# Optimization experiments

Hardware: AMD Instinct MI355X
Metric: run time of the kernel (lower is better)

Reference implementation:

```python
import jax, jax.numpy as jnp
import numpy as np

D_MODEL = 1024
NUM_HEADS = 16
D_K = D_MODEL // NUM_HEADS

def setup_inputs() -> dict:
    key = jax.random.key(0)
    ks = jax.random.split(key, 8)
    B, S, D = 2, 2048, D_MODEL
    scale = 1.0 / np.sqrt(D)
    return {
        "X_q": jax.random.normal(ks[0], (B, S, D), dtype=jnp.float32),
        "X_k": jax.random.normal(ks[1], (B, S, D), dtype=jnp.float32),
        "X_v": jax.random.normal(ks[2], (B, S, D), dtype=jnp.float32),
        "W_q": jax.random.normal(ks[3], (D, D), dtype=jnp.float32) * scale,
        "W_k": jax.random.normal(ks[4], (D, D), dtype=jnp.float32) * scale,
        "W_v": jax.random.normal(ks[5], (D, D), dtype=jnp.float32) * scale,
        "W_o": jax.random.normal(ks[6], (D, D), dtype=jnp.float32) * scale,
        "b_o": jnp.zeros((D,), dtype=jnp.float32),
    }

def reference(X_q, X_k, X_v, W_q, W_k, W_v, W_o, b_o):
    B, S, D = X_q.shape
    H, dk = NUM_HEADS, D_K
    # nn.Linear: x @ W.T
    Q = (X_q @ W_q.T).reshape(B, H, S, dk)  # faithful raw view, no transpose
    K = (X_k @ W_k.T).reshape(B, H, S, dk)
    V = (X_v @ W_v.T).reshape(B, H, S, dk)
    A = jnp.einsum("bhqd,bhkd->bhqk", Q, K) / np.sqrt(dk)  # [B,H,S,S]
    A = jax.nn.softmax(A, axis=-1)
    H_cat = jnp.einsum("bhqk,bhkd->bhqd", A, V).reshape(B, S, D)
    return H_cat @ W_o.T + b_o
```

## Files before the change

### kernel.cpp

```cpp
#include <hip/hip_runtime.h>

typedef __bf16 bf16;
typedef bf16 bf16x8 __attribute__((ext_vector_type(8)));
typedef bf16 bf16x4 __attribute__((ext_vector_type(4)));
typedef bf16 bf16x2 __attribute__((ext_vector_type(2)));
typedef float f32x4 __attribute__((ext_vector_type(4)));
typedef float f32x16 __attribute__((ext_vector_type(16)));
typedef int i32x4 __attribute__((ext_vector_type(4)));

#define XSZ 4194304
#define WSZ 1048576
#define KDIM 1024
#define QSCALE 0.1803368801111137f

__device__ __forceinline__ void async16(const bf16* g, bf16* l) {
  __builtin_amdgcn_global_load_lds(
      (const __attribute__((address_space(1))) unsigned int*)g,
      (__attribute__((address_space(3))) unsigned int*)l, 16, 0, 0);
}

__device__ __forceinline__ bf16x8 ld8(const bf16* p) {
  bf16x4 lo = *(const bf16x4*)p;
  bf16x4 hi = *(const bf16x4*)(p + 4);
  return __builtin_shufflevector(lo, hi, 0, 1, 2, 3, 4, 5, 6, 7);
}

__device__ __forceinline__ void st8s(bf16* p, bf16x8 v) {
  *(bf16x4*)p       = __builtin_shufflevector(v, v, 0, 1, 2, 3);
  *(bf16x4*)(p + 4) = __builtin_shufflevector(v, v, 4, 5, 6, 7);
}

__device__ __forceinline__ f32x4 mfma16(bf16x8 a, bf16x8 b, f32x4 c) {
  return __builtin_amdgcn_mfma_f32_16x16x32_bf16(a, b, c, 0, 0, 0);
}
__device__ __forceinline__ f32x16 mfma32(bf16x8 a, bf16x8 b, f32x16 c) {
  return __builtin_amdgcn_mfma_f32_32x32x16_bf16(a, b, c, 0, 0, 0);
}

__device__ __forceinline__ int packbf2(float lo, float hi) {
  bf16x2 t; t[0] = (bf16)lo; t[1] = (bf16)hi;
  return __builtin_bit_cast(int, t);
}

__device__ __forceinline__ float fast_exp2(float x) {
#if __has_builtin(__builtin_amdgcn_exp2f)
  return __builtin_amdgcn_exp2f(x);
#else
  return exp2f(x);
#endif
}

__global__ __launch_bounds__(256) void cast_all(const float* __restrict__ Xq, const float* __restrict__ Xk,
                                                const float* __restrict__ Xv, const float* __restrict__ Wq,
                                                const float* __restrict__ Wk, const float* __restrict__ Wv,
                                                const float* __restrict__ Wo, bf16* __restrict__ dst) {
  size_t i = ((size_t)blockIdx.x * 256 + threadIdx.x) * 8;
  const float* src; size_t off; float scale = 1.0f;
  if (i < XSZ)                { src = Xq; off = i; }
  else if (i < 2 * (size_t)XSZ) { src = Xk; off = i - XSZ; }
  else if (i < 3 * (size_t)XSZ) { src = Xv; off = i - 2 * (size_t)XSZ; }
  else if (i < 3 * (size_t)XSZ + WSZ) { src = Wq; off = i - 3 * (size_t)XSZ; scale = QSCALE; }
  else if (i < 3 * (size_t)XSZ + 2 * (size_t)WSZ) { src = Wk; off = i - 3 * (size_t)XSZ - WSZ; }
  else if (i < 3 * (size_t)XSZ + 3 * (size_t)WSZ) { src = Wv; off = i - 3 * (size_t)XSZ - 2 * (size_t)WSZ; }
  else                        { src = Wo; off = i - 3 * (size_t)XSZ - 3 * (size_t)WSZ; }
  float4 a = *(const float4*)(src + off);
  float4 b = *(const float4*)(src + off + 4);
  bf16x8 o;
  o[0] = (bf16)(a.x * scale); o[1] = (bf16)(a.y * scale);
  o[2] = (bf16)(a.z * scale); o[3] = (bf16)(a.w * scale);
  o[4] = (bf16)(b.x * scale); o[5] = (bf16)(b.y * scale);
  o[6] = (bf16)(b.z * scale); o[7] = (bf16)(b.w * scale);
  *(bf16x8*)(dst + i) = o;
}

__device__ __forceinline__ void gemm_nt_core(const bf16* __restrict__ A, const bf16* __restrict__ Bm,
                                             int m0, int n0, bf16* lds, f32x4 acc[4][4]) {
  const int t = threadIdx.x;
  const int lane = t & 63, wave = t >> 6;
  const int wm = wave & 1, wn = wave >> 1;
  const int quad = lane >> 4, m16 = lane & 15;
  bf16* As = lds;
  bf16* Bs = lds + 128 * 32;
  const int c0 = t, c1 = t + 256;
  const bf16* ga0 = A + (size_t)(m0 + (c0 >> 2)) * KDIM + (c0 & 3) * 8;
  const bf16* ga1 = A + (size_t)(m0 + (c1 >> 2)) * KDIM + (c1 & 3) * 8;
  const bf16* gb0 = Bm + (size_t)(n0 + (c0 >> 2)) * KDIM + (c0 & 3) * 8;
  const bf16* gb1 = Bm + (size_t)(n0 + (c1 >> 2)) * KDIM + (c1 & 3) * 8;
  for (int kt = 0; kt < KDIM; kt += 32) {
    async16(ga0 + kt, As + c0 * 8);
    async16(ga1 + kt, As + c1 * 8);
    async16(gb0 + kt, Bs + c0 * 8);
    async16(gb1 + kt, Bs + c1 * 8);
    __syncthreads();
    bf16x8 af[4], bfv[4];
    #pragma unroll
    for (int i = 0; i < 4; i++)
      af[i] = *(const bf16x8*)(As + (wm * 64 + i * 16 + m16) * 32 + quad * 8);
    #pragma unroll
    for (int i = 0; i < 4; i++)
      bfv[i] = *(const bf16x8*)(Bs + (wn * 64 + i * 16 + m16) * 32 + quad * 8);
    #pragma unroll
    for (int mi = 0; mi < 4; mi++)
      #pragma unroll
      for (int ni = 0; ni < 4; ni++)
        acc[mi][ni] = mfma16(af[mi], bfv[ni], acc[mi][ni]);
    __syncthreads();
  }
}

__global__ __launch_bounds__(256) void proj_gemm(const bf16* __restrict__ xq, const bf16* __restrict__ xk,
                                                 const bf16* __restrict__ xv, const bf16* __restrict__ wq,
                                                 const bf16* __restrict__ wk, const bf16* __restrict__ wv,
                                                 bf16* __restrict__ Qo, bf16* __restrict__ Ko,
                                                 bf16* __restrict__ Vo) {
  __shared__ bf16 lds[2 * 128 * 32];
  const int z = blockIdx.z;
  const bf16* A = (z == 0) ? xq : (z == 1) ? xk : xv;
  const bf16* W = (z == 0) ? wq : (z == 1) ? wk : wv;
  bf16* C = (z == 0) ? Qo : (z == 1) ? Ko : Vo;
  f32x4 acc[4][4];
  #pragma unroll
  for (int i = 0; i < 4; i++)
    #pragma unroll
    for (int j = 0; j < 4; j++) acc[i][j] = (f32x4){0.f, 0.f, 0.f, 0.f};
  gemm_nt_core(A, W, blockIdx.y * 128, blockIdx.x * 128, lds, acc);
  const int lane = threadIdx.x & 63, wave = threadIdx.x >> 6;
  const int wm = wave & 1, wn = wave >> 1, quad = lane >> 4, m16 = lane & 15;
  const int row0 = blockIdx.y * 128 + wm * 64;
  const int col0 = blockIdx.x * 128 + wn * 64;
  #pragma unroll
  for (int mi = 0; mi < 4; mi++)
    #pragma unroll
    for (int ni = 0; ni < 4; ni++)
      #pragma unroll
      for (int r = 0; r < 4; r++) {
        int row = row0 + mi * 16 + quad * 4 + r;
        int col = col0 + ni * 16 + m16;
        C[(size_t)row * 1024 + col] = (bf16)acc[mi][ni][r];
      }
}

__global__ __launch_bounds__(256) void out_gemm(const bf16* __restrict__ Hm, const bf16* __restrict__ wo,
                                                const float* __restrict__ bias, float* __restrict__ out) {
  __shared__ bf16 lds[128 * 32 + 64 * 32];
  bf16* As = lds;
  bf16* Bs = lds + 128 * 32;
  const int t = threadIdx.x;
  const int lane = t & 63, wave = t >> 6;
  const int wm = wave & 1, wn = wave >> 1;
  const int quad = lane >> 4, m16 = lane & 15;
  const int m0 = blockIdx.y * 128, n0 = blockIdx.x * 64;
  const int c0 = t, c1 = t + 256;
  const bf16* ga0 = Hm + (size_t)(m0 + (c0 >> 2)) * KDIM + (c0 & 3) * 8;
  const bf16* ga1 = Hm + (size_t)(m0 + (c1 >> 2)) * KDIM + (c1 & 3) * 8;
  const bf16* gb0 = wo + (size_t)(n0 + (c0 >> 2)) * KDIM + (c0 & 3) * 8;
  f32x4 acc[4][2];
  #pragma unroll
  for (int i = 0; i < 4; i++)
    #pragma unroll
    for (int j = 0; j < 2; j++) acc[i][j] = (f32x4){0.f, 0.f, 0.f, 0.f};
  for (int kt = 0; kt < KDIM; kt += 32) {
    async16(ga0 + kt, As + c0 * 8);
    async16(ga1 + kt, As + c1 * 8);
    if (c0 < 256) async16(gb0 + kt, Bs + c0 * 8);
    __syncthreads();
    bf16x8 af[4], bfv[2];
    #pragma unroll
    for (int i = 0; i < 4; i++)
      af[i] = *(const bf16x8*)(As + (wm * 64 + i * 16 + m16) * 32 + quad * 8);
    #pragma unroll
    for (int i = 0; i < 2; i++)
      bfv[i] = *(const bf16x8*)(Bs + (wn * 32 + i * 16 + m16) * 32 + quad * 8);
    #pragma unroll
    for (int mi = 0; mi < 4; mi++)
      #pragma unroll
      for (int ni = 0; ni < 2; ni++)
        acc[mi][ni] = mfma16(af[mi], bfv[ni], acc[mi][ni]);
    __syncthreads();
  }
  const int row0 = m0 + wm * 64;
  const int col0 = n0 + wn * 32;
  float bv[2];
  #pragma unroll
  for (int ni = 0; ni < 2; ni++) bv[ni] = bias[col0 + ni * 16 + m16];
  #pragma unroll
  for (int mi = 0; mi < 4; mi++)
    #pragma unroll
    for (int ni = 0; ni < 2; ni++)
      #pragma unroll
      for (int r = 0; r < 4; r++) {
        int row = row0 + mi * 16 + quad * 4 + r;
        int col = col0 + ni * 16 + m16;
        out[(size_t)row * 1024 + col] = acc[mi][ni][r] + bv[ni];
      }
}

__global__ __launch_bounds__(256) void transpose_v(const bf16* __restrict__ V, bf16* __restrict__ Vt) {
  __shared__ bf16 T[64 * 65];
  const int t = threadIdx.x;
  const bf16* src = V + (size_t)blockIdx.y * (2048 * 64) + (size_t)blockIdx.x * 64 * 64;
  bf16* dst = Vt + (size_t)blockIdx.y * (2048 * 64) + (size_t)blockIdx.x * 64;
  #pragma unroll
  for (int j = 0; j < 2; j++) {
    int c = t + j * 256;
    int row = c >> 3, col8 = (c & 7) * 8;
    bf16x8 v = *(const bf16x8*)(src + row * 64 + col8);
    #pragma unroll
    for (int i = 0; i < 8; i++) T[row * 65 + col8 + i] = v[i];
  }
  __syncthreads();
  #pragma unroll
  for (int j = 0; j < 2; j++) {
    int c = t + j * 256;
    int d = c >> 3, k8 = (c & 7) * 8;
    bf16x8 o;
    #pragma unroll
    for (int i = 0; i < 8; i++) o[i] = T[(k8 + i) * 65 + d];
    *(bf16x8*)(dst + (size_t)d * 2048 + k8) = o;
  }
}

#define KS 68
#define VS 132
__global__ __launch_bounds__(256, 3) void attn_kernel(const bf16* __restrict__ Qg,
                                                      const bf16* __restrict__ Kg,
                                                      const bf16* __restrict__ Vtg,
                                                      float* __restrict__ U0,
                                                      float* __restrict__ l0) {
  __shared__ bf16 smem[128 * KS + 64 * VS];
  bf16* Ks = smem;
  bf16* Vs = smem + 128 * KS;
  const int t = threadIdx.x;
  const int lane = t & 63, w = t >> 6;
  const int l31 = lane & 31, h = lane >> 5;
  const int L = blockIdx.x + 16 * (blockIdx.y + 32 * blockIdx.z);
  const int xcd = L & 7, j5 = L >> 3;
  const int bh = xcd * 4 + (j5 & 3);
  const int slab = (j5 >> 2) & 1;
  const int qt = j5 >> 3;
  const size_t base = (size_t)bh * (2048 * 64);
  const bf16* Kp = Kg + base + (size_t)slab * (1024 * 64);
  const bf16* Vp = Vtg + base + slab * 1024;
  float* U = U0 + (size_t)slab * (32 * 131072) + (size_t)bh * 131072;
  float* lv = l0 + slab * (32 * 2048) + bh * 2048;
  const int q = qt * 128 + w * 32 + l31;

  bf16x8 qf[4];
  #pragma unroll
  for (int kc = 0; kc < 4; kc++)
    qf[kc] = *(const bf16x8*)(Qg + base + (size_t)q * 64 + 16 * kc + 8 * h);

  f32x16 oacc[2];
  #pragma unroll
  for (int mt = 0; mt < 2; mt++)
    #pragma unroll
    for (int i = 0; i < 16; i++) oacc[mt][i] = 0.f;
  float lrow = 0.f;

  int krow[4], kcol[4], vrow[4], vcol[4];
  #pragma unroll
  for (int j = 0; j < 4; j++) {
    int c = t + j * 256;
    krow[j] = c >> 3;  kcol[j] = (c & 7) * 8;
    vrow[j] = c >> 4;  vcol[j] = (c & 15) * 8;
  }

  bf16x8 kreg[4], vreg[4];
  #pragma unroll
  for (int j = 0; j < 4; j++) {
    kreg[j] = *(const bf16x8*)(Kp + (size_t)krow[j] * 64 + kcol[j]);
    vreg[j] = *(const bf16x8*)(Vp + (size_t)vrow[j] * 2048 + vcol[j]);
  }

  for (int kt = 0; kt < 8; kt++) {
    #pragma unroll
    for (int j = 0; j < 4; j++) st8s(Ks + krow[j] * KS + kcol[j], kreg[j]);
    #pragma unroll
    for (int j = 0; j < 4; j++) st8s(Vs + vrow[j] * VS + vcol[j], vreg[j]);
    __syncthreads();

    if (kt + 1 < 8) {
      #pragma unroll
      for (int j = 0; j < 4; j++) {
        kreg[j] = *(const bf16x8*)(Kp + (size_t)((kt + 1) * 128 + krow[j]) * 64 + kcol[j]);
        vreg[j] = *(const bf16x8*)(Vp + (size_t)vrow[j] * 2048 + (kt + 1) * 128 + vcol[j]);
      }
    }

    #pragma unroll
    for (int mt = 0; mt < 4; mt++) {
      f32x16 sacc;
      #pragma unroll
      for (int i = 0; i < 16; i++) sacc[i] = 0.f;
      #pragma unroll
      for (int kc = 0; kc < 4; kc++) {
        bf16x8 kf = ld8(Ks + (32 * mt + l31) * KS + 16 * kc + 8 * h);
        sacc = mfma32(kf, qf[kc], sacc);
      }
      int pd[8];
      float sum = 0.f;
      #pragma unroll
      for (int p = 0; p < 8; p++) {
        float p0 = fast_exp2(sacc[2 * p]);
        float p1 = fast_exp2(sacc[2 * p + 1]);
        sum += p0 + p1;
        pd[p] = packbf2(p0, p1);
      }
      lrow += sum;
      #pragma unroll
      for (int c1 = 0; c1 < 2; c1++) {
        const int kc = 2 * mt + c1;
        const int rro = 2 * c1 + h;
        const int rrp = 2 * c1 + 1 - h;
        int s0 = __shfl_xor(pd[2 * rrp], 32, 64);
        int s1 = __shfl_xor(pd[2 * rrp + 1], 32, 64);
        int o0 = pd[2 * rro], o1 = pd[2 * rro + 1];
        i32x4 w4;
        w4.x = h ? s0 : o0;
        w4.y = h ? s1 : o1;
        w4.z = h ? o0 : s0;
        w4.w = h ? o1 : s1;
        bf16x8 pfrag = __builtin_bit_cast(bf16x8, w4);
        #pragma unroll
        for (int mtd = 0; mtd < 2; mtd++) {
          bf16x8 vf = ld8(Vs + (32 * mtd + l31) * VS + 16 * kc + 8 * h);
          oacc[mtd] = mfma32(vf, pfrag, oacc[mtd]);
        }
      }
    }
    __syncthreads();
  }

  lrow += __shfl_xor(lrow, 32, 64);
  #pragma unroll
  for (int mt = 0; mt < 2; mt++)
    #pragma unroll
    for (int r = 0; r < 16; r++) {
      int d = 32 * mt + (r & 3) + 8 * (r >> 2) + 4 * h;
      U[(size_t)d * 2048 + q] = oacc[mt][r];
    }
  if (h == 0) lv[q] = lrow;
}

__global__ __launch_bounds__(256) void merge_kernel(const float* __restrict__ Ua,
                                                    const float* __restrict__ Ub,
                                                    const float* __restrict__ la,
                                                    const float* __restrict__ lb,
                                                    bf16* __restrict__ H) {
  __shared__ float T[64 * 65];
  const int t = threadIdx.x;
  const int q0 = blockIdx.x * 64;
  const int bh = blockIdx.y;
  const float* A = Ua + (size_t)bh * 131072;
  const float* Bp = Ub + (size_t)bh * 131072;
  #pragma unroll
  for (int p = 0; p < 4; p++) {
    int d = p * 16 + (t >> 4);
    int qq = (t & 15) * 4;
    f32x4 a = *(const f32x4*)(A + (size_t)d * 2048 + q0 + qq);
    f32x4 b = *(const f32x4*)(Bp + (size_t)d * 2048 + q0 + qq);
    #pragma unroll
    for (int i = 0; i < 4; i++) T[d * 65 + qq + i] = a[i] + b[i];
  }
  __syncthreads();
  const float* lap = la + bh * 2048 + q0;
  const float* lbp = lb + bh * 2048 + q0;
  #pragma unroll
  for (int p = 0; p < 2; p++) {
    int ql = p * 32 + (t >> 3);
    int d8 = (t & 7) * 8;
    float inv = 1.f / (lap[ql] + lbp[ql]);
    bf16x8 o;
    #pragma unroll
    for (int i = 0; i < 8; i++) o[i] = (bf16)(T[(d8 + i) * 65 + ql] * inv);
    *(bf16x8*)(H + (size_t)bh * 131072 + (size_t)(q0 + ql) * 64 + d8) = o;
  }
}

extern "C" void kernel_launch(void* const* d_in, const int* in_sizes, int n_in,
                              void* d_out, int out_size, void* d_ws, size_t ws_size,
                              hipStream_t stream) {
  const float* Xq = (const float*)d_in[0];
  const float* Xk = (const float*)d_in[1];
  const float* Xv = (const float*)d_in[2];
  const float* Wq = (const float*)d_in[3];
  const float* Wk = (const float*)d_in[4];
  const float* Wv = (const float*)d_in[5];
  const float* Wo = (const float*)d_in[6];
  const float* bo = (const float*)d_in[7];

  bf16* ws = (bf16*)d_ws;
  bf16* xq = ws;
  bf16* xk = ws + XSZ;
  bf16* xv = ws + 2 * (size_t)XSZ;
  bf16* wq = ws + 3 * (size_t)XSZ;
  bf16* wk = wq + WSZ;
  bf16* wv = wk + WSZ;
  bf16* wo = wv + WSZ;
  bf16* q  = wo + WSZ;
  bf16* k  = q + XSZ;
  bf16* v  = k + XSZ;
  bf16* vt = xv;
  bf16* h  = xq;
  float* U0  = (float*)v;
  float* l0f = (float*)xk;

  cast_all<<<8192, 256, 0, stream>>>(Xq, Xk, Xv, Wq, Wk, Wv, Wo, ws);
  proj_gemm<<<dim3(8, 32, 3), 256, 0, stream>>>(xq, xk, xv, wq, wk, wv, q, k, v);
  transpose_v<<<dim3(32, 32), 256, 0, stream>>>(v, vt);
  attn_kernel<<<dim3(16, 32, 2), 256, 0, stream>>>(q, k, vt, U0, l0f);
  merge_kernel<<<dim3(32, 32), 256, 0, stream>>>(U0, U0 + 32 * 131072, l0f, l0f + 65536, h);
  out_gemm<<<dim3(16, 32), 256, 0, stream>>>(h, wo, bo, (float*)d_out);
}
```

Baseline: 257.1 us.

## Process two query tiles per attention block to reuse K/V shared-memory tiles

Each attention block now handles 256 queries (two 128-query groups) instead of 128, so every K/V tile staged in LDS and every K/V fragment loaded into registers feeds twice as many MFMAs. The grid is halved and launch bounds drop from 3 to 2 blocks per CU to allow the larger register footprint. The intent is to cut global and LDS traffic per unit of compute, at the cost of fewer blocks (1024 vs 512 per slab set) and lower occupancy, which could hurt latency hiding.

```diff
diff --git a/kernel.cpp b/kernel.cpp
--- a/kernel.cpp
+++ b/kernel.cpp
@@ -222,7 +222,7 @@
 
 #define KS 68
 #define VS 132
-__global__ __launch_bounds__(256, 3) void attn_kernel(const bf16* __restrict__ Qg,
+__global__ __launch_bounds__(256, 2) void attn_kernel(const bf16* __restrict__ Qg,
                                                       const bf16* __restrict__ Kg,
                                                       const bf16* __restrict__ Vtg,
                                                       float* __restrict__ U0,
@@ -233,7 +233,7 @@
   const int t = threadIdx.x;
   const int lane = t & 63, w = t >> 6;
   const int l31 = lane & 31, h = lane >> 5;
-  const int L = blockIdx.x + 16 * (blockIdx.y + 32 * blockIdx.z);
+  const int L = blockIdx.x + 8 * (blockIdx.y + 32 * blockIdx.z);
   const int xcd = L & 7, j5 = L >> 3;
   const int bh = xcd * 4 + (j5 & 3);
   const int slab = (j5 >> 2) & 1;
@@ -243,19 +243,24 @@
   const bf16* Vp = Vtg + base + slab * 1024;
   float* U = U0 + (size_t)slab * (32 * 131072) + (size_t)bh * 131072;
   float* lv = l0 + slab * (32 * 2048) + bh * 2048;
-  const int q = qt * 128 + w * 32 + l31;
-
-  bf16x8 qf[4];
-  #pragma unroll
-  for (int kc = 0; kc < 4; kc++)
-    qf[kc] = *(const bf16x8*)(Qg + base + (size_t)q * 64 + 16 * kc + 8 * h);
-
-  f32x16 oacc[2];
-  #pragma unroll
-  for (int mt = 0; mt < 2; mt++)
-    #pragma unroll
-    for (int i = 0; i < 16; i++) oacc[mt][i] = 0.f;
-  float lrow = 0.f;
+  const int qc0 = qt * 256 + w * 32 + l31;
+  const int qc1 = qc0 + 128;
+
+  bf16x8 qf[2][4];
+  #pragma unroll
+  for (int kc = 0; kc < 4; kc++) {
+    qf[0][kc] = *(const bf16x8*)(Qg + base + (size_t)qc0 * 64 + 16 * kc + 8 * h);
+    qf[1][kc] = *(const bf16x8*)(Qg + base + (size_t)qc1 * 64 + 16 * kc + 8 * h);
+  }
+
+  f32x16 oacc[2][2];
+  #pragma unroll
+  for (int g = 0; g < 2; g++)
+    #pragma unroll
+    for (int mtd = 0; mtd < 2; mtd++)
+      #pragma unroll
+      for (int i = 0; i < 16; i++) oacc[g][mtd][i] = 0.f;
+  float lrow[2] = {0.f, 0.f};
 
   int krow[4], kcol[4], vrow[4], vcol[4];
   #pragma unroll
@@ -289,57 +294,69 @@
 
     #pragma unroll
     for (int mt = 0; mt < 4; mt++) {
-      f32x16 sacc;
-      #pragma unroll
-      for (int i = 0; i < 16; i++) sacc[i] = 0.f;
+      bf16x8 kf[4];
+      #pragma unroll
+      for (int kc = 0; kc < 4; kc++)
+        kf[kc] = ld8(Ks + (32 * mt + l31) * KS + 16 * kc + 8 * h);
+      f32x16 s0, s1;
+      #pragma unroll
+      for (int i = 0; i < 16; i++) { s0[i] = 0.f; s1[i] = 0.f; }
       #pragma unroll
       for (int kc = 0; kc < 4; kc++) {
-        bf16x8 kf = ld8(Ks + (32 * mt + l31) * KS + 16 * kc + 8 * h);
-        sacc = mfma32(kf, qf[kc], sacc);
-      }
-      int pd[8];
-      float sum = 0.f;
+        s0 = mfma32(kf[kc], qf[0][kc], s0);
+        s1 = mfma32(kf[kc], qf[1][kc], s1);
+      }
+      int pd[2][8];
+      float sum0 = 0.f, sum1 = 0.f;
       #pragma unroll
       for (int p = 0; p < 8; p++) {
-        float p0 = fast_exp2(sacc[2 * p]);
-        float p1 = fast_exp2(sacc[2 * p + 1]);
-        sum += p0 + p1;
-        pd[p] = packbf2(p0, p1);
-      }
-      lrow += sum;
+        float a0 = fast_exp2(s0[2 * p]), a1 = fast_exp2(s0[2 * p + 1]);
+        sum0 += a0 + a1;
+        pd[0][p] = packbf2(a0, a1);
+        float b0 = fast_exp2(s1[2 * p]), b1 = fast_exp2(s1[2 * p + 1]);
+        sum1 += b0 + b1;
+        pd[1][p] = packbf2(b0, b1);
+      }
+      lrow[0] += sum0; lrow[1] += sum1;
       #pragma unroll
       for (int c1 = 0; c1 < 2; c1++) {
         const int kc = 2 * mt + c1;
+        bf16x8 vf0 = ld8(Vs + (size_t)l31 * VS + 16 * kc + 8 * h);
+        bf16x8 vf1 = ld8(Vs + (size_t)(32 + l31) * VS + 16 * kc + 8 * h);
         const int rro = 2 * c1 + h;
         const int rrp = 2 * c1 + 1 - h;
-        int s0 = __shfl_xor(pd[2 * rrp], 32, 64);
-        int s1 = __shfl_xor(pd[2 * rrp + 1], 32, 64);
-        int o0 = pd[2 * rro], o1 = pd[2 * rro + 1];
-        i32x4 w4;
-        w4.x = h ? s0 : o0;
-        w4.y = h ? s1 : o1;
-        w4.z = h ? o0 : s0;
-        w4.w = h ? o1 : s1;
-        bf16x8 pfrag = __builtin_bit_cast(bf16x8, w4);
         #pragma unroll
-        for (int mtd = 0; mtd < 2; mtd++) {
-          bf16x8 vf = ld8(Vs + (32 * mtd + l31) * VS + 16 * kc + 8 * h);
-          oacc[mtd] = mfma32(vf, pfrag, oacc[mtd]);
+        for (int g = 0; g < 2; g++) {
+          int sw0 = __shfl_xor(pd[g][2 * rrp], 32, 64);
+          int sw1 = __shfl_xor(pd[g][2 * rrp + 1], 32, 64);
+          int o0 = pd[g][2 * rro], o1 = pd[g][2 * rro + 1];
+          i32x4 w4;
+          w4.x = h ? sw0 : o0;
+          w4.y = h ? sw1 : o1;
+          w4.z = h ? o0 : sw0;
+          w4.w = h ? o1 : sw1;
+          bf16x8 pfrag = __builtin_bit_cast(bf16x8, w4);
+          oacc[g][0] = mfma32(vf0, pfrag, oacc[g][0]);
+          oacc[g][1] = mfma32(vf1, pfrag, oacc[g][1]);
         }
       }
     }
     __syncthreads();
   }
 
-  lrow += __shfl_xor(lrow, 32, 64);
-  #pragma unroll
-  for (int mt = 0; mt < 2; mt++)
-    #pragma unroll
-    for (int r = 0; r < 16; r++) {
-      int d = 32 * mt + (r & 3) + 8 * (r >> 2) + 4 * h;
-      U[(size_t)d * 2048 + q] = oacc[mt][r];
-    }
-  if (h == 0) lv[q] = lrow;
+  #pragma unroll
+  for (int g = 0; g < 2; g++) {
+    int q = g ? qc1 : qc0;
+    float lr = lrow[g] + __shfl_xor(lrow[g], 32, 64);
+    #pragma unroll
+    for (int mtd = 0; mtd < 2; mtd++)
+      #pragma unroll
+      for (int r = 0; r < 16; r++) {
+        int d = 32 * mtd + (r & 3) + 8 * (r >> 2) + 4 * h;
+        U[(size_t)d * 2048 + q] = oacc[g][mtd][r];
+      }
+    if (h == 0) lv[q] = lr;
+  }
 }
 
 __global__ __launch_bounds__(256) void merge_kernel(const float* __restrict__ Ua,
@@ -408,7 +425,7 @@
   cast_all<<<8192, 256, 0, stream>>>(Xq, Xk, Xv, Wq, Wk, Wv, Wo, ws);
   proj_gemm<<<dim3(8, 32, 3), 256, 0, stream>>>(xq, xk, xv, wq, wk, wv, q, k, v);
   transpose_v<<<dim3(32, 32), 256, 0, stream>>>(v, vt);
-  attn_kernel<<<dim3(16, 32, 2), 256, 0, stream>>>(q, k, vt, U0, l0f);
+  attn_kernel<<<dim3(8, 32, 2), 256, 0, stream>>>(q, k, vt, U0, l0f);
   merge_kernel<<<dim3(32, 32), 256, 0, stream>>>(U0, U0 + 32 * 131072, l0f, l0f + 65536, h);
   out_gemm<<<dim3(16, 32), 256, 0, stream>>>(h, wo, bo, (float*)d_out);
 }
```

Measured after the change: 299.9 us. 16.6% more time.

## Drop split-K attention and fuse normalization epilogue, removing merge kernel

Applied to the files above, without the earlier changes.

Each attention block now walks all 2048 keys instead of half, normalizes by the row sum in-kernel, and writes the bf16 head output directly through a shared-memory transpose. This eliminates the fp32 partial-output buffers and the separate merge kernel with its global-memory round trip and launch. In exchange, the grid halves to 512 blocks, which lowers parallelism and may underfill the CUs, and each block's serial loop doubles in length.

```diff
diff --git a/kernel.cpp b/kernel.cpp
--- a/kernel.cpp
+++ b/kernel.cpp
@@ -225,24 +225,20 @@
 __global__ __launch_bounds__(256, 3) void attn_kernel(const bf16* __restrict__ Qg,
                                                       const bf16* __restrict__ Kg,
                                                       const bf16* __restrict__ Vtg,
-                                                      float* __restrict__ U0,
-                                                      float* __restrict__ l0) {
+                                                      bf16* __restrict__ Hout) {
   __shared__ bf16 smem[128 * KS + 64 * VS];
   bf16* Ks = smem;
   bf16* Vs = smem + 128 * KS;
   const int t = threadIdx.x;
   const int lane = t & 63, w = t >> 6;
   const int l31 = lane & 31, h = lane >> 5;
-  const int L = blockIdx.x + 16 * (blockIdx.y + 32 * blockIdx.z);
+  const int L = blockIdx.x + 16 * blockIdx.y;
   const int xcd = L & 7, j5 = L >> 3;
   const int bh = xcd * 4 + (j5 & 3);
-  const int slab = (j5 >> 2) & 1;
-  const int qt = j5 >> 3;
+  const int qt = j5 >> 2;
   const size_t base = (size_t)bh * (2048 * 64);
-  const bf16* Kp = Kg + base + (size_t)slab * (1024 * 64);
-  const bf16* Vp = Vtg + base + slab * 1024;
-  float* U = U0 + (size_t)slab * (32 * 131072) + (size_t)bh * 131072;
-  float* lv = l0 + slab * (32 * 2048) + bh * 2048;
+  const bf16* Kp = Kg + base;
+  const bf16* Vp = Vtg + base;
   const int q = qt * 128 + w * 32 + l31;
 
   bf16x8 qf[4];
@@ -272,14 +268,14 @@
     vreg[j] = *(const bf16x8*)(Vp + (size_t)vrow[j] * 2048 + vcol[j]);
   }
 
-  for (int kt = 0; kt < 8; kt++) {
+  for (int kt = 0; kt < 16; kt++) {
     #pragma unroll
     for (int j = 0; j < 4; j++) st8s(Ks + krow[j] * KS + kcol[j], kreg[j]);
     #pragma unroll
     for (int j = 0; j < 4; j++) st8s(Vs + vrow[j] * VS + vcol[j], vreg[j]);
     __syncthreads();
 
-    if (kt + 1 < 8) {
+    if (kt + 1 < 16) {
       #pragma unroll
       for (int j = 0; j < 4; j++) {
         kreg[j] = *(const bf16x8*)(Kp + (size_t)((kt + 1) * 128 + krow[j]) * 64 + kcol[j]);
@@ -332,48 +328,23 @@
   }
 
   lrow += __shfl_xor(lrow, 32, 64);
+  float inv = 1.f / lrow;
+  float* Tf = (float*)smem + w * 2048;
   #pragma unroll
   for (int mt = 0; mt < 2; mt++)
     #pragma unroll
     for (int r = 0; r < 16; r++) {
       int d = 32 * mt + (r & 3) + 8 * (r >> 2) + 4 * h;
-      U[(size_t)d * 2048 + q] = oacc[mt][r];
+      Tf[d * 32 + l31] = oacc[mt][r] * inv;
     }
-  if (h == 0) lv[q] = lrow;
-}
-
-__global__ __launch_bounds__(256) void merge_kernel(const float* __restrict__ Ua,
-                                                    const float* __restrict__ Ub,
-                                                    const float* __restrict__ la,
-                                                    const float* __restrict__ lb,
-                                                    bf16* __restrict__ H) {
-  __shared__ float T[64 * 65];
-  const int t = threadIdx.x;
-  const int q0 = blockIdx.x * 64;
-  const int bh = blockIdx.y;
-  const float* A = Ua + (size_t)bh * 131072;
-  const float* Bp = Ub + (size_t)bh * 131072;
-  #pragma unroll
-  for (int p = 0; p < 4; p++) {
-    int d = p * 16 + (t >> 4);
-    int qq = (t & 15) * 4;
-    f32x4 a = *(const f32x4*)(A + (size_t)d * 2048 + q0 + qq);
-    f32x4 b = *(const f32x4*)(Bp + (size_t)d * 2048 + q0 + qq);
-    #pragma unroll
-    for (int i = 0; i < 4; i++) T[d * 65 + qq + i] = a[i] + b[i];
-  }
   __syncthreads();
-  const float* lap = la + bh * 2048 + q0;
-  const float* lbp = lb + bh * 2048 + q0;
-  #pragma unroll
-  for (int p = 0; p < 2; p++) {
-    int ql = p * 32 + (t >> 3);
-    int d8 = (t & 7) * 8;
-    float inv = 1.f / (lap[ql] + lbp[ql]);
+  bf16* Hq = Hout + base + (size_t)(qt * 128 + w * 32 + l31) * 64 + 32 * h;
+  #pragma unroll
+  for (int s = 0; s < 4; s++) {
     bf16x8 o;
     #pragma unroll
-    for (int i = 0; i < 8; i++) o[i] = (bf16)(T[(d8 + i) * 65 + ql] * inv);
-    *(bf16x8*)(H + (size_t)bh * 131072 + (size_t)(q0 + ql) * 64 + d8) = o;
+    for (int i = 0; i < 8; i++) o[i] = (bf16)Tf[(32 * h + s * 8 + i) * 32 + l31];
+    *(bf16x8*)(Hq + s * 8) = o;
   }
 }
 
@@ -402,13 +373,10 @@
   bf16* v  = k + XSZ;
   bf16* vt = xv;
   bf16* h  = xq;
-  float* U0  = (float*)v;
-  float* l0f = (float*)xk;
 
   cast_all<<<8192, 256, 0, stream>>>(Xq, Xk, Xv, Wq, Wk, Wv, Wo, ws);
   proj_gemm<<<dim3(8, 32, 3), 256, 0, stream>>>(xq, xk, xv, wq, wk, wv, q, k, v);
   transpose_v<<<dim3(32, 32), 256, 0, stream>>>(v, vt);
-  attn_kernel<<<dim3(16, 32, 2), 256, 0, stream>>>(q, k, vt, U0, l0f);
-  merge_kernel<<<dim3(32, 32), 256, 0, stream>>>(U0, U0 + 32 * 131072, l0f, l0f + 65536, h);
+  attn_kernel<<<dim3(16, 32), 256, 0, stream>>>(q, k, vt, h);
   out_gemm<<<dim3(16, 32), 256, 0, stream>>>(h, wo, bo, (float*)d_out);
 }
```

Result: no change. 254.4 us (-1.1%).
